# Kernel optimization log

Measured on AMD Instinct MI355X. Metric: run time of the kernel, lower is better.

Reference implementation:

```python
import jax, jax.numpy as jnp
import numpy as np

B, H, N, D = 16, 8, 256, 32


def setup_inputs() -> dict:
    key = jax.random.key(0)
    k1, k2, k3 = jax.random.split(key, 3)
    q = jax.random.normal(k1, (B, H, N, D), dtype=jnp.float32)
    k = jax.random.normal(k2, (B, H, N, D), dtype=jnp.float32)
    scale = jnp.ones((1,), dtype=jnp.float32)  # unused by the module
    mask = jnp.zeros((B, 1, N, N), dtype=bool)  # True == masked out
    # learned attention vector, xavier_uniform over (1, H, 1, 1, D)
    fan = 1 * H * 1 * 1 * D
    bound = float(np.sqrt(6.0 / (1 + D)))  # xavier for (..., D) param
    attention = jax.random.uniform(k3, (1, H, 1, 1, D), dtype=jnp.float32,
                                   minval=-bound, maxval=bound)
    return {"q": q, "k": k, "scale": scale, "mask": mask, "attention": attention}


def reference(q, k, scale, mask, attention):
    # summed: [B, H, Nq, Nk, D] via broadcast of q.unsqueeze(-2)+k.unsqueeze(-3)
    summed = q[:, :, :, None, :] + k[:, :, None, :, :]
    # GATv2 score: a^T * silu(q_i + k_j), reduced over head_dim
    scores = jnp.sum(jax.nn.silu(summed) * attention, axis=-1)  # [B, H, Nq, Nk]
    neg = jnp.finfo(scores.dtype).min
    scores_masked = jnp.where(mask, neg, scores)
    attn = jax.nn.softmax(scores_masked, axis=-1)
    return attn
```

## Files before the change

kernel.cpp:

```cpp
#include <hip/hip_runtime.h>
#include <stdint.h>
#include <stddef.h>

constexpr int Bc = 16, Hc = 8, Nc = 256, Dc = 32;
constexpr float LOG2E = 1.44269504088896340736f;

constexpr int    MF    = 10;
constexpr double PHALF = 9.7;
constexpr double LFIT  = 9.0;

constexpr double PI_ = 3.14159265358979323846;

constexpr double cexp_(double x) {
    int n = (int)(x >= 0 ? x + 0.5 : x - 0.5);
    double f = x - n, t = 1.0, s = 1.0;
    for (int i = 1; i <= 26; ++i) { t *= f / i; s += t; }
    const double E = 2.71828182845904523536;
    double en = 1.0, bb = n >= 0 ? E : 1.0 / E;
    int an = n < 0 ? -n : n;
    for (int i = 0; i < an; ++i) en *= bb;
    return s * en;
}
constexpr double creduce_(double x) {
    while (x >  PI_) x -= 2.0 * PI_;
    while (x < -PI_) x += 2.0 * PI_;
    return x;
}
constexpr double ccos_(double x0) {
    double x = creduce_(x0), x2 = x * x, t = 1.0, s = 1.0;
    for (int i = 1; i <= 16; ++i) { t *= -x2 / ((2.0*i - 1.0) * (2.0*i)); s += t; }
    return s;
}
constexpr double csin_(double x0) {
    double x = creduce_(x0), x2 = x * x, t = x, s = x;
    for (int i = 1; i <= 16; ++i) { t *= -x2 / ((2.0*i) * (2.0*i + 1.0)); s += t; }
    return s;
}
constexpr double Gfun_(double x) {
    double z = x < 0 ? -x : x;
    double e = cexp_(z);
    return 0.5 * z * ((e - 1.0) / (e + 1.0));
}
constexpr double csqrt_(double x) {
    if (x <= 0) return 0;
    double r = x > 1 ? x : 1;
    for (int i = 0; i < 40; ++i) r = 0.5 * (r + x / r);
    return r;
}

struct FitT { float tk[MF + 1]; float tq[MF + 1]; };

constexpr FitT lsFit_() {
    constexpr int NB = MF + 1;
    double A[NB][NB] = {}, bv[NB] = {};
    for (int p = 0; p < NB; ++p)
        for (int qq = 0; qq < NB; ++qq) {
            double wm = (p - qq) * PI_ / PHALF, wp = (p + qq) * PI_ / PHALF;
            double Sm = (p == qq)     ? LFIT : csin_(wm * LFIT) / wm;
            double Sp = (p + qq == 0) ? LFIT : csin_(wp * LFIT) / wp;
            A[p][qq] = 0.5 * (Sm + Sp);
        }
    constexpr int NS = 128;
    double hh = LFIT / NS, gx[NS + 1] = {};
    for (int i = 0; i <= NS; ++i) gx[i] = Gfun_(i * hh);
    for (int p = 0; p < NB; ++p) {
        double s = 0;
        for (int i = 0; i <= NS; ++i) {
            double wgt = (i == 0 || i == NS) ? 1.0 : ((i & 1) ? 4.0 : 2.0);
            s += wgt * gx[i] * ccos_(p * PI_ / PHALF * (i * hh));
        }
        bv[p] = s * hh / 3.0;
    }
    for (int p = 0; p < NB; ++p) A[p][p] += 1e-8 * LFIT;
    for (int col = 0; col < NB; ++col) {
        int piv = col; double best = A[col][col] < 0 ? -A[col][col] : A[col][col];
        for (int r = col + 1; r < NB; ++r) {
            double v = A[r][col] < 0 ? -A[r][col] : A[r][col];
            if (v > best) { best = v; piv = r; }
        }
        if (piv != col) {
            for (int cc = 0; cc < NB; ++cc) { double t = A[col][cc]; A[col][cc] = A[piv][cc]; A[piv][cc] = t; }
            double t = bv[col]; bv[col] = bv[piv]; bv[piv] = t;
        }
        for (int r = col + 1; r < NB; ++r) {
            double f = A[r][col] / A[col][col];
            for (int cc = col; cc < NB; ++cc) A[r][cc] -= f * A[col][cc];
            bv[r] -= f * bv[col];
        }
    }
    double c[NB] = {};
    for (int r = NB - 1; r >= 0; --r) {
        double s = bv[r];
        for (int cc = r + 1; cc < NB; ++cc) s -= A[r][cc] * c[cc];
        c[r] = s / A[r][r];
    }
    FitT f{};
    for (int m = 0; m <= MF; ++m) {
        double rt = csqrt_(c[m] < 0 ? -c[m] : c[m]);
        f.tk[m] = (float)rt;
        f.tq[m] = (float)(c[m] < 0 ? -rt : rt);
    }
    return f;
}
constexpr FitT CF = lsFit_();

typedef _Float16 half8  __attribute__((ext_vector_type(8)));
typedef float    f32x16 __attribute__((ext_vector_type(16)));

__device__ __forceinline__ uint32_t pkh_(float a, float b) {
    auto v = __builtin_amdgcn_cvt_pkrtz(a, b);
    uint32_t u; __builtin_memcpy(&u, &v, 4); return u;
}

constexpr int ROWB = 144;
constexpr int KB_  = Nc * ROWB;
constexpr int QB_  = 128 * ROWB;
constexpr int BUF  = KB_ + QB_;
constexpr int SRED_OFF = 2 * BUF;
constexpr int AKV_OFF  = SRED_OFF + 2048;
constexpr int SMEM     = AKV_OFF + 1024;

__global__ __launch_bounds__(512, 2) void gatv2_mfma_kernel(
    const float* __restrict__ q, const float* __restrict__ k,
    const uint8_t* __restrict__ mask, const float* __restrict__ att,
    float* __restrict__ out)
{
    extern __shared__ char smem[];
    float* sred = (float*)(smem + SRED_OFF);
    float* akv  = (float*)(smem + AKV_OFF);

    const int tid = threadIdx.x, lane = tid & 63, w = tid >> 6;
    const int bh = blockIdx.y, h = bh & 7, b = bh >> 3;
    const int iBlk = blockIdx.x * 128;
    const float invTwoP = (float)(1.0 / (2.0 * PHALF));

    const int dq = tid & 7, rw = tid >> 3;
    const float4 a4 = *(const float4*)(att + h * Dc + 4 * dq);

    const float* kbase = k + (size_t)bh * Nc * Dc;
    float kc1[16], ks1[16], kcm[16], ksm[16];
    int offK[4];
#pragma unroll
    for (int it = 0; it < 4; ++it) {
        const int j = rw + it * 64;
        const float4 kv = *(const float4*)(kbase + j * Dc + 4 * dq);
        float part = a4.x * kv.x + a4.y * kv.y + a4.z * kv.z + a4.w * kv.w;
        part += __shfl_xor(part, 1, 64);
        part += __shfl_xor(part, 2, 64);
        part += __shfl_xor(part, 4, 64);
        if (dq == 0) akv[j] = part;
        const float rv[4] = { kv.x, kv.y, kv.z, kv.w };
#pragma unroll
        for (int c = 0; c < 4; ++c) {
            float r = __builtin_amdgcn_fractf(rv[c] * invTwoP);
            kc1[4*it+c] = __builtin_amdgcn_cosf(r);
            ks1[4*it+c] = __builtin_amdgcn_sinf(r);
            kcm[4*it+c] = kc1[4*it+c];
            ksm[4*it+c] = ks1[4*it+c];
        }
        offK[it] = j * ROWB + dq * 16;
    }
    const float* qbase = q + ((size_t)bh * Nc + iBlk) * Dc;
    float qc1[8], qs1[8], qcm[8], qsm[8];
    int offQ[2];
#pragma unroll
    for (int it = 0; it < 2; ++it) {
        const int iq = rw + it * 64;
        const float4 qv = *(const float4*)(qbase + iq * Dc + 4 * dq);
        const float rv[4] = { qv.x, qv.y, qv.z, qv.w };
#pragma unroll
        for (int c = 0; c < 4; ++c) {
            float r = __builtin_amdgcn_fractf(rv[c] * invTwoP);
            qc1[4*it+c] = __builtin_amdgcn_cosf(r);
            qs1[4*it+c] = __builtin_amdgcn_sinf(r);
            qcm[4*it+c] = qc1[4*it+c];
            qsm[4*it+c] = qs1[4*it+c];
        }
        offQ[it] = KB_ + iq * ROWB + dq * 16;
    }

    const int hi5 = lane >> 5, col = lane & 31;
    const int wi = w & 1, wj = w >> 1;
    const int baseA0 = KB_ + (wi * 64 + col) * ROWB, baseA1 = baseA0 + 32 * ROWB;
    const int baseB0 = (wj * 64 + col) * ROWB,       baseB1 = baseB0 + 32 * ROWB;

    f32x16 acc[2][2];
#pragma unroll
    for (int i2 = 0; i2 < 2; ++i2)
#pragma unroll
        for (int j2 = 0; j2 < 2; ++j2)
#pragma unroll
            for (int e = 0; e < 16; ++e) acc[i2][j2][e] = 0.0f;

    auto buildWrite = [&](int mN, int dstOff) {
        const float tk = CF.tk[mN];
        const float g0 = CF.tq[mN]*a4.x, g1 = CF.tq[mN]*a4.y;
        const float g2 = CF.tq[mN]*a4.z, g3 = CF.tq[mN]*a4.w;
#pragma unroll
        for (int it = 0; it < 4; ++it) {
            uint4 wv;
            wv.x = pkh_(tk * kcm[4*it+0], tk * ksm[4*it+0]);
            wv.y = pkh_(tk * kcm[4*it+1], tk * ksm[4*it+1]);
            wv.z = pkh_(tk * kcm[4*it+2], tk * ksm[4*it+2]);
            wv.w = pkh_(tk * kcm[4*it+3], tk * ksm[4*it+3]);
            *(uint4*)(smem + dstOff + offK[it]) = wv;
        }
#pragma unroll
        for (int it = 0; it < 2; ++it) {
            uint4 wv;
            wv.x = pkh_(g0 * qcm[4*it+0], -(g0 * qsm[4*it+0]));
            wv.y = pkh_(g1 * qcm[4*it+1], -(g1 * qsm[4*it+1]));
            wv.z = pkh_(g2 * qcm[4*it+2], -(g2 * qsm[4*it+2]));
            wv.w = pkh_(g3 * qcm[4*it+3], -(g3 * qsm[4*it+3]));
            *(uint4*)(smem + dstOff + offQ[it]) = wv;
        }
    };
    auto rotate = [&]() {
#pragma unroll
        for (int e = 0; e < 16; ++e) {
            float cn = fmaf(kc1[e], kcm[e], -(ks1[e] * ksm[e]));
            float sn = fmaf(ks1[e], kcm[e],   kc1[e] * ksm[e]);
            kcm[e] = cn; ksm[e] = sn;
        }
#pragma unroll
        for (int e = 0; e < 8; ++e) {
            float cn = fmaf(qc1[e], qcm[e], -(qs1[e] * qsm[e]));
            float sn = fmaf(qs1[e], qcm[e],   qc1[e] * qsm[e]);
            qcm[e] = cn; qsm[e] = sn;
        }
    };
    auto loadFrags = [&](int srcOff, int s, half8& A0, half8& A1,
                         half8& B0, half8& B1) {
        const int du = (2 * s + hi5) << 4;
        A0 = *(const half8*)(smem + srcOff + baseA0 + du);
        A1 = *(const half8*)(smem + srcOff + baseA1 + du);
        B0 = *(const half8*)(smem + srcOff + baseB0 + du);
        B1 = *(const half8*)(smem + srcOff + baseB1 + du);
    };
    auto mfma4 = [&](half8 A0, half8 A1, half8 B0, half8 B1) {
        acc[0][0] = __builtin_amdgcn_mfma_f32_32x32x16_f16(A0, B0, acc[0][0], 0, 0, 0);
        acc[0][1] = __builtin_amdgcn_mfma_f32_32x32x16_f16(A0, B1, acc[0][1], 0, 0, 0);
        acc[1][0] = __builtin_amdgcn_mfma_f32_32x32x16_f16(A1, B0, acc[1][0], 0, 0, 0);
        acc[1][1] = __builtin_amdgcn_mfma_f32_32x32x16_f16(A1, B1, acc[1][1], 0, 0, 0);
    };

    buildWrite(1, 0);
    rotate();
    __syncthreads();
#pragma unroll
    for (int m = 1; m <= MF; ++m) {
        const int srcOff = ((m - 1) & 1) * BUF;
        const int dstOff = (m & 1) * BUF;
        half8 A0a, A1a, B0a, B1a, A0b, A1b, B0b, B1b;
        loadFrags(srcOff, 0, A0a, A1a, B0a, B1a);
        loadFrags(srcOff, 1, A0b, A1b, B0b, B1b);
        if (m < MF) { buildWrite(m + 1, dstOff); rotate(); }
        __builtin_amdgcn_s_setprio(1);
        mfma4(A0a, A1a, B0a, B1a);
        loadFrags(srcOff, 2, A0a, A1a, B0a, B1a);
        mfma4(A0b, A1b, B0b, B1b);
        loadFrags(srcOff, 3, A0b, A1b, B0b, B1b);
        mfma4(A0a, A1a, B0a, B1a);
        mfma4(A0b, A1b, B0b, B1b);
        __builtin_amdgcn_s_setprio(0);
        if (m < MF) __syncthreads();
    }

    constexpr float M0 = 24.0f;
    const int jB = wj * 64;
    const float akj0 = akv[jB + col], akj1 = akv[jB + 32 + col];
    const int iB = iBlk + wi * 64;

#pragma unroll
    for (int i2 = 0; i2 < 2; ++i2) {
        float v[16];
#pragma unroll
        for (int e = 0; e < 16; ++e) {
            const int rloc = (e & 3) + 8 * (e >> 2) + 4 * hi5;
            const int ig = iB + i2 * 32 + rloc;
            const uint8_t* mr = mask + ((size_t)(b * Nc + ig)) * Nc + jB + col;
            const uint8_t m0 = mr[0], m1 = mr[32];
            float v0 = fmaf(0.5f, akj0, acc[i2][0][e]);
            float v1 = fmaf(0.5f, akj1, acc[i2][1][e]);
            float p0 = __builtin_amdgcn_exp2f(__builtin_fminf((v0 - M0) * LOG2E, 80.0f));
            float p1 = __builtin_amdgcn_exp2f(__builtin_fminf((v1 - M0) * LOG2E, 80.0f));
            if (m0) p0 = 0.0f;
            if (m1) p1 = 0.0f;
            acc[i2][0][e] = p0;
            acc[i2][1][e] = p1;
            v[e] = p0 + p1;
        }
        float u8[8];
#pragma unroll
        for (int jj = 0; jj < 8; ++jj) {
            float mn = (col & 16) ? v[jj + 8] : v[jj];
            float sd = (col & 16) ? v[jj]     : v[jj + 8];
            u8[jj] = mn + __shfl_xor(sd, 16, 64);
        }
        float u4[4];
#pragma unroll
        for (int jj = 0; jj < 4; ++jj) {
            float mn = (col & 8) ? u8[jj + 4] : u8[jj];
            float sd = (col & 8) ? u8[jj]     : u8[jj + 4];
            u4[jj] = mn + __shfl_xor(sd, 8, 64);
        }
        float u2[2];
#pragma unroll
        for (int jj = 0; jj < 2; ++jj) {
            float mn = (col & 4) ? u4[jj + 2] : u4[jj];
            float sd = (col & 4) ? u4[jj]     : u4[jj + 2];
            u2[jj] = mn + __shfl_xor(sd, 4, 64);
        }
        float t1;
        {
            float mn = (col & 2) ? u2[1] : u2[0];
            float sd = (col & 2) ? u2[0] : u2[1];
            t1 = mn + __shfl_xor(sd, 2, 64);
        }
        t1 += __shfl_xor(t1, 1, 64);
        {
            const int eL = ((col & 16) ? 8 : 0) + ((col & 8) ? 4 : 0)
                         + ((col & 4) ? 2 : 0) + ((col & 2) ? 1 : 0);
            const int rl = (eL & 3) + 8 * (eL >> 2) + 4 * hi5;
            if (!(col & 1)) sred[(wi * 64 + i2 * 32 + rl) * 4 + wj] = t1;
        }
    }
    __syncthreads();

    float* obase = out + (size_t)bh * Nc * Nc;
#pragma unroll
    for (int i2 = 0; i2 < 2; ++i2)
#pragma unroll
    for (int e = 0; e < 16; ++e) {
        const int rloc = (e & 3) + 8 * (e >> 2) + 4 * hi5;
        const int iL = wi * 64 + i2 * 32 + rloc;
        const int ig = iBlk + iL;
        const float4 tv = *(const float4*)(&sred[iL * 4]);
        const float inv = __builtin_amdgcn_rcpf(tv.x + tv.y + tv.z + tv.w);
        obase[(size_t)ig * Nc + jB + col]      = acc[i2][0][e] * inv;
        obase[(size_t)ig * Nc + jB + 32 + col] = acc[i2][1][e] * inv;
    }
}

extern "C" void kernel_launch(void* const* d_in, const int* in_sizes, int n_in,
                              void* d_out, int out_size, void* d_ws, size_t ws_size,
                              hipStream_t stream) {
    const float*   q    = (const float*)d_in[0];
    const float*   k    = (const float*)d_in[1];
    const uint8_t* mask = (const uint8_t*)d_in[3];
    const float*   att  = (const float*)d_in[4];
    float*         out  = (float*)d_out;

    (void)hipFuncSetAttribute((const void*)gatv2_mfma_kernel,
                              hipFuncAttributeMaxDynamicSharedMemorySize, SMEM);

    dim3 grid(2, Bc * Hc);
    dim3 block(512);
    gatv2_mfma_kernel<<<grid, block, SMEM, stream>>>(q, k, mask, att, out);
}
```

Measured before the change: 91.38 us.

## Split block into producer waves building Fourier features and MFMA consumer waves

Adds four producer waves to each block (768 threads). The producers compute the cos/sin feature tiles for every harmonic and write them into the double-buffered LDS, while the original eight waves only run the MFMA loop and the softmax epilogue. The producers no longer advance the features with the incremental angle-rotation recurrence; they recompute cos/sin directly from a stored phase on each harmonic. The aim is to take feature generation off the MFMA waves' critical path. In exchange it raises the thread count and register pressure under launch_bounds(768,3), uses more transcendental instructions, and still synchronises with a block barrier on every harmonic.

```diff
diff --git a/kernel.cpp b/kernel.cpp
--- a/kernel.cpp
+++ b/kernel.cpp
@@ -120,7 +120,7 @@
 constexpr int AKV_OFF  = SRED_OFF + 2048;
 constexpr int SMEM     = AKV_OFF + 1024;
 
-__global__ __launch_bounds__(512, 2) void gatv2_mfma_kernel(
+__global__ __launch_bounds__(768, 3) void gatv2_mfma_kernel(
     const float* __restrict__ q, const float* __restrict__ k,
     const uint8_t* __restrict__ mask, const float* __restrict__ att,
     float* __restrict__ out)
@@ -133,100 +133,94 @@
     const int bh = blockIdx.y, h = bh & 7, b = bh >> 3;
     const int iBlk = blockIdx.x * 128;
     const float invTwoP = (float)(1.0 / (2.0 * PHALF));
-
-    const int dq = tid & 7, rw = tid >> 3;
-    const float4 a4 = *(const float4*)(att + h * Dc + 4 * dq);
-
-    const float* kbase = k + (size_t)bh * Nc * Dc;
-    float kc1[16], ks1[16], kcm[16], ksm[16];
-    int offK[4];
-#pragma unroll
-    for (int it = 0; it < 4; ++it) {
-        const int j = rw + it * 64;
-        const float4 kv = *(const float4*)(kbase + j * Dc + 4 * dq);
-        float part = a4.x * kv.x + a4.y * kv.y + a4.z * kv.z + a4.w * kv.w;
-        part += __shfl_xor(part, 1, 64);
-        part += __shfl_xor(part, 2, 64);
-        part += __shfl_xor(part, 4, 64);
-        if (dq == 0) akv[j] = part;
-        const float rv[4] = { kv.x, kv.y, kv.z, kv.w };
-#pragma unroll
-        for (int c = 0; c < 4; ++c) {
-            float r = __builtin_amdgcn_fractf(rv[c] * invTwoP);
-            kc1[4*it+c] = __builtin_amdgcn_cosf(r);
-            ks1[4*it+c] = __builtin_amdgcn_sinf(r);
-            kcm[4*it+c] = kc1[4*it+c];
-            ksm[4*it+c] = ks1[4*it+c];
-        }
-        offK[it] = j * ROWB + dq * 16;
-    }
-    const float* qbase = q + ((size_t)bh * Nc + iBlk) * Dc;
-    float qc1[8], qs1[8], qcm[8], qsm[8];
-    int offQ[2];
-#pragma unroll
-    for (int it = 0; it < 2; ++it) {
-        const int iq = rw + it * 64;
-        const float4 qv = *(const float4*)(qbase + iq * Dc + 4 * dq);
-        const float rv[4] = { qv.x, qv.y, qv.z, qv.w };
-#pragma unroll
-        for (int c = 0; c < 4; ++c) {
-            float r = __builtin_amdgcn_fractf(rv[c] * invTwoP);
-            qc1[4*it+c] = __builtin_amdgcn_cosf(r);
-            qs1[4*it+c] = __builtin_amdgcn_sinf(r);
-            qcm[4*it+c] = qc1[4*it+c];
-            qsm[4*it+c] = qs1[4*it+c];
-        }
-        offQ[it] = KB_ + iq * ROWB + dq * 16;
-    }
+    const bool isProd = (w >= 8);
+
+    float kph[32], qph[16];
+    int offK[8], offQ[4];
+    float4 a4p{0,0,0,0};
 
     const int hi5 = lane >> 5, col = lane & 31;
-    const int wi = w & 1, wj = w >> 1;
+    const int wi = w & 1, wj = (w >> 1) & 3;
     const int baseA0 = KB_ + (wi * 64 + col) * ROWB, baseA1 = baseA0 + 32 * ROWB;
     const int baseB0 = (wj * 64 + col) * ROWB,       baseB1 = baseB0 + 32 * ROWB;
 
     f32x16 acc[2][2];
-#pragma unroll
-    for (int i2 = 0; i2 < 2; ++i2)
-#pragma unroll
-        for (int j2 = 0; j2 < 2; ++j2)
-#pragma unroll
-            for (int e = 0; e < 16; ++e) acc[i2][j2][e] = 0.0f;
+
+    if (isProd) {
+        const int p = tid - 512, dq = p & 7, rw = p >> 3;
+        a4p = *(const float4*)(att + h * Dc + 4 * dq);
+        const float* kbase = k + (size_t)bh * Nc * Dc;
+#pragma unroll
+        for (int it = 0; it < 8; ++it) {
+            const int j = rw + it * 32;
+            const float4 kv = *(const float4*)(kbase + j * Dc + 4 * dq);
+            float part = a4p.x * kv.x + a4p.y * kv.y + a4p.z * kv.z + a4p.w * kv.w;
+            part += __shfl_xor(part, 1, 64);
+            part += __shfl_xor(part, 2, 64);
+            part += __shfl_xor(part, 4, 64);
+            if (dq == 0) akv[j] = part;
+            kph[4*it+0] = __builtin_amdgcn_fractf(kv.x * invTwoP);
+            kph[4*it+1] = __builtin_amdgcn_fractf(kv.y * invTwoP);
+            kph[4*it+2] = __builtin_amdgcn_fractf(kv.z * invTwoP);
+            kph[4*it+3] = __builtin_amdgcn_fractf(kv.w * invTwoP);
+            offK[it] = j * ROWB + dq * 16;
+        }
+        const float* qbase = q + ((size_t)bh * Nc + iBlk) * Dc;
+#pragma unroll
+        for (int it = 0; it < 4; ++it) {
+            const int iq = rw + it * 32;
+            const float4 qv = *(const float4*)(qbase + iq * Dc + 4 * dq);
+            qph[4*it+0] = __builtin_amdgcn_fractf(qv.x * invTwoP);
+            qph[4*it+1] = __builtin_amdgcn_fractf(qv.y * invTwoP);
+            qph[4*it+2] = __builtin_amdgcn_fractf(qv.z * invTwoP);
+            qph[4*it+3] = __builtin_amdgcn_fractf(qv.w * invTwoP);
+            offQ[it] = KB_ + iq * ROWB + dq * 16;
+        }
+    } else {
+#pragma unroll
+        for (int i2 = 0; i2 < 2; ++i2)
+#pragma unroll
+            for (int j2 = 0; j2 < 2; ++j2)
+#pragma unroll
+                for (int e = 0; e < 16; ++e) acc[i2][j2][e] = 0.0f;
+    }
 
     auto buildWrite = [&](int mN, int dstOff) {
+        const float mf = (float)mN;
         const float tk = CF.tk[mN];
-        const float g0 = CF.tq[mN]*a4.x, g1 = CF.tq[mN]*a4.y;
-        const float g2 = CF.tq[mN]*a4.z, g3 = CF.tq[mN]*a4.w;
+        const float g0 = CF.tq[mN]*a4p.x, g1 = CF.tq[mN]*a4p.y;
+        const float g2 = CF.tq[mN]*a4p.z, g3 = CF.tq[mN]*a4p.w;
+#pragma unroll
+        for (int it = 0; it < 8; ++it) {
+            float cs[4], sn[4];
+#pragma unroll
+            for (int c = 0; c < 4; ++c) {
+                const float r = __builtin_amdgcn_fractf(mf * kph[4*it+c]);
+                cs[c] = __builtin_amdgcn_cosf(r);
+                sn[c] = __builtin_amdgcn_sinf(r);
+            }
+            uint4 wv;
+            wv.x = pkh_(tk * cs[0], tk * sn[0]);
+            wv.y = pkh_(tk * cs[1], tk * sn[1]);
+            wv.z = pkh_(tk * cs[2], tk * sn[2]);
+            wv.w = pkh_(tk * cs[3], tk * sn[3]);
+            *(uint4*)(smem + dstOff + offK[it]) = wv;
+        }
 #pragma unroll
         for (int it = 0; it < 4; ++it) {
+            float cs[4], sn[4];
+#pragma unroll
+            for (int c = 0; c < 4; ++c) {
+                const float r = __builtin_amdgcn_fractf(mf * qph[4*it+c]);
+                cs[c] = __builtin_amdgcn_cosf(r);
+                sn[c] = __builtin_amdgcn_sinf(r);
+            }
             uint4 wv;
-            wv.x = pkh_(tk * kcm[4*it+0], tk * ksm[4*it+0]);
-            wv.y = pkh_(tk * kcm[4*it+1], tk * ksm[4*it+1]);
-            wv.z = pkh_(tk * kcm[4*it+2], tk * ksm[4*it+2]);
-            wv.w = pkh_(tk * kcm[4*it+3], tk * ksm[4*it+3]);
-            *(uint4*)(smem + dstOff + offK[it]) = wv;
-        }
-#pragma unroll
-        for (int it = 0; it < 2; ++it) {
-            uint4 wv;
-            wv.x = pkh_(g0 * qcm[4*it+0], -(g0 * qsm[4*it+0]));
-            wv.y = pkh_(g1 * qcm[4*it+1], -(g1 * qsm[4*it+1]));
-            wv.z = pkh_(g2 * qcm[4*it+2], -(g2 * qsm[4*it+2]));
-            wv.w = pkh_(g3 * qcm[4*it+3], -(g3 * qsm[4*it+3]));
+            wv.x = pkh_(g0 * cs[0], -(g0 * sn[0]));
+            wv.y = pkh_(g1 * cs[1], -(g1 * sn[1]));
+            wv.z = pkh_(g2 * cs[2], -(g2 * sn[2]));
+            wv.w = pkh_(g3 * cs[3], -(g3 * sn[3]));
             *(uint4*)(smem + dstOff + offQ[it]) = wv;
-        }
-    };
-    auto rotate = [&]() {
-#pragma unroll
-        for (int e = 0; e < 16; ++e) {
-            float cn = fmaf(kc1[e], kcm[e], -(ks1[e] * ksm[e]));
-            float sn = fmaf(ks1[e], kcm[e],   kc1[e] * ksm[e]);
-            kcm[e] = cn; ksm[e] = sn;
-        }
-#pragma unroll
-        for (int e = 0; e < 8; ++e) {
-            float cn = fmaf(qc1[e], qcm[e], -(qs1[e] * qsm[e]));
-            float sn = fmaf(qs1[e], qcm[e],   qc1[e] * qsm[e]);
-            qcm[e] = cn; qsm[e] = sn;
         }
     };
     auto loadFrags = [&](int srcOff, int s, half8& A0, half8& A1,
@@ -244,101 +238,106 @@
         acc[1][1] = __builtin_amdgcn_mfma_f32_32x32x16_f16(A1, B1, acc[1][1], 0, 0, 0);
     };
 
-    buildWrite(1, 0);
-    rotate();
+    if (isProd) buildWrite(1, 0);
     __syncthreads();
 #pragma unroll
     for (int m = 1; m <= MF; ++m) {
-        const int srcOff = ((m - 1) & 1) * BUF;
-        const int dstOff = (m & 1) * BUF;
-        half8 A0a, A1a, B0a, B1a, A0b, A1b, B0b, B1b;
-        loadFrags(srcOff, 0, A0a, A1a, B0a, B1a);
-        loadFrags(srcOff, 1, A0b, A1b, B0b, B1b);
-        if (m < MF) { buildWrite(m + 1, dstOff); rotate(); }
-        __builtin_amdgcn_s_setprio(1);
-        mfma4(A0a, A1a, B0a, B1a);
-        loadFrags(srcOff, 2, A0a, A1a, B0a, B1a);
-        mfma4(A0b, A1b, B0b, B1b);
-        loadFrags(srcOff, 3, A0b, A1b, B0b, B1b);
-        mfma4(A0a, A1a, B0a, B1a);
-        mfma4(A0b, A1b, B0b, B1b);
-        __builtin_amdgcn_s_setprio(0);
+        if (!isProd) {
+            const int srcOff = ((m - 1) & 1) * BUF;
+            half8 A0a, A1a, B0a, B1a, A0b, A1b, B0b, B1b;
+            loadFrags(srcOff, 0, A0a, A1a, B0a, B1a);
+            loadFrags(srcOff, 1, A0b, A1b, B0b, B1b);
+            __builtin_amdgcn_s_setprio(1);
+            mfma4(A0a, A1a, B0a, B1a);
+            loadFrags(srcOff, 2, A0a, A1a, B0a, B1a);
+            mfma4(A0b, A1b, B0b, B1b);
+            loadFrags(srcOff, 3, A0b, A1b, B0b, B1b);
+            mfma4(A0a, A1a, B0a, B1a);
+            mfma4(A0b, A1b, B0b, B1b);
+            __builtin_amdgcn_s_setprio(0);
+        } else if (m < MF) {
+            buildWrite(m + 1, (m & 1) * BUF);
+        }
         if (m < MF) __syncthreads();
     }
 
     constexpr float M0 = 24.0f;
     const int jB = wj * 64;
-    const float akj0 = akv[jB + col], akj1 = akv[jB + 32 + col];
     const int iB = iBlk + wi * 64;
 
-#pragma unroll
-    for (int i2 = 0; i2 < 2; ++i2) {
-        float v[16];
+    if (!isProd) {
+        const float akj0 = akv[jB + col], akj1 = akv[jB + 32 + col];
+#pragma unroll
+        for (int i2 = 0; i2 < 2; ++i2) {
+            float v[16];
+#pragma unroll
+            for (int e = 0; e < 16; ++e) {
+                const int rloc = (e & 3) + 8 * (e >> 2) + 4 * hi5;
+                const int ig = iB + i2 * 32 + rloc;
+                const uint8_t* mr = mask + ((size_t)(b * Nc + ig)) * Nc + jB + col;
+                const uint8_t m0 = mr[0], m1 = mr[32];
+                float v0 = fmaf(0.5f, akj0, acc[i2][0][e]);
+                float v1 = fmaf(0.5f, akj1, acc[i2][1][e]);
+                float p0 = __builtin_amdgcn_exp2f(__builtin_fminf((v0 - M0) * LOG2E, 80.0f));
+                float p1 = __builtin_amdgcn_exp2f(__builtin_fminf((v1 - M0) * LOG2E, 80.0f));
+                if (m0) p0 = 0.0f;
+                if (m1) p1 = 0.0f;
+                acc[i2][0][e] = p0;
+                acc[i2][1][e] = p1;
+                v[e] = p0 + p1;
+            }
+            float u8[8];
+#pragma unroll
+            for (int jj = 0; jj < 8; ++jj) {
+                float mn = (col & 16) ? v[jj + 8] : v[jj];
+                float sd = (col & 16) ? v[jj]     : v[jj + 8];
+                u8[jj] = mn + __shfl_xor(sd, 16, 64);
+            }
+            float u4[4];
+#pragma unroll
+            for (int jj = 0; jj < 4; ++jj) {
+                float mn = (col & 8) ? u8[jj + 4] : u8[jj];
+                float sd = (col & 8) ? u8[jj]     : u8[jj + 4];
+                u4[jj] = mn + __shfl_xor(sd, 8, 64);
+            }
+            float u2[2];
+#pragma unroll
+            for (int jj = 0; jj < 2; ++jj) {
+                float mn = (col & 4) ? u4[jj + 2] : u4[jj];
+                float sd = (col & 4) ? u4[jj]     : u4[jj + 2];
+                u2[jj] = mn + __shfl_xor(sd, 4, 64);
+            }
+            float t1;
+            {
+                float mn = (col & 2) ? u2[1] : u2[0];
+                float sd = (col & 2) ? u2[0] : u2[1];
+                t1 = mn + __shfl_xor(sd, 2, 64);
+            }
+            t1 += __shfl_xor(t1, 1, 64);
+            {
+                const int eL = ((col & 16) ? 8 : 0) + ((col & 8) ? 4 : 0)
+                             + ((col & 4) ? 2 : 0) + ((col & 2) ? 1 : 0);
+                const int rl = (eL & 3) + 8 * (eL >> 2) + 4 * hi5;
+                if (!(col & 1)) sred[(wi * 64 + i2 * 32 + rl) * 4 + wj] = t1;
+            }
+        }
+    }
+    __syncthreads();
+
+    if (!isProd) {
+        float* obase = out + (size_t)bh * Nc * Nc;
+#pragma unroll
+        for (int i2 = 0; i2 < 2; ++i2)
 #pragma unroll
         for (int e = 0; e < 16; ++e) {
             const int rloc = (e & 3) + 8 * (e >> 2) + 4 * hi5;
-            const int ig = iB + i2 * 32 + rloc;
-            const uint8_t* mr = mask + ((size_t)(b * Nc + ig)) * Nc + jB + col;
-            const uint8_t m0 = mr[0], m1 = mr[32];
-            float v0 = fmaf(0.5f, akj0, acc[i2][0][e]);
-            float v1 = fmaf(0.5f, akj1, acc[i2][1][e]);
-            float p0 = __builtin_amdgcn_exp2f(__builtin_fminf((v0 - M0) * LOG2E, 80.0f));
-            float p1 = __builtin_amdgcn_exp2f(__builtin_fminf((v1 - M0) * LOG2E, 80.0f));
-            if (m0) p0 = 0.0f;
-            if (m1) p1 = 0.0f;
-            acc[i2][0][e] = p0;
-            acc[i2][1][e] = p1;
-            v[e] = p0 + p1;
-        }
-        float u8[8];
-#pragma unroll
-        for (int jj = 0; jj < 8; ++jj) {
-            float mn = (col & 16) ? v[jj + 8] : v[jj];
-            float sd = (col & 16) ? v[jj]     : v[jj + 8];
-            u8[jj] = mn + __shfl_xor(sd, 16, 64);
-        }
-        float u4[4];
-#pragma unroll
-        for (int jj = 0; jj < 4; ++jj) {
-            float mn = (col & 8) ? u8[jj + 4] : u8[jj];
-            float sd = (col & 8) ? u8[jj]     : u8[jj + 4];
-            u4[jj] = mn + __shfl_xor(sd, 8, 64);
-        }
-        float u2[2];
-#pragma unroll
-        for (int jj = 0; jj < 2; ++jj) {
-            float mn = (col & 4) ? u4[jj + 2] : u4[jj];
-            float sd = (col & 4) ? u4[jj]     : u4[jj + 2];
-            u2[jj] = mn + __shfl_xor(sd, 4, 64);
-        }
-        float t1;
-        {
-            float mn = (col & 2) ? u2[1] : u2[0];
-            float sd = (col & 2) ? u2[0] : u2[1];
-            t1 = mn + __shfl_xor(sd, 2, 64);
-        }
-        t1 += __shfl_xor(t1, 1, 64);
-        {
-            const int eL = ((col & 16) ? 8 : 0) + ((col & 8) ? 4 : 0)
-                         + ((col & 4) ? 2 : 0) + ((col & 2) ? 1 : 0);
-            const int rl = (eL & 3) + 8 * (eL >> 2) + 4 * hi5;
-            if (!(col & 1)) sred[(wi * 64 + i2 * 32 + rl) * 4 + wj] = t1;
-        }
-    }
-    __syncthreads();
-
-    float* obase = out + (size_t)bh * Nc * Nc;
-#pragma unroll
-    for (int i2 = 0; i2 < 2; ++i2)
-#pragma unroll
-    for (int e = 0; e < 16; ++e) {
-        const int rloc = (e & 3) + 8 * (e >> 2) + 4 * hi5;
-        const int iL = wi * 64 + i2 * 32 + rloc;
-        const int ig = iBlk + iL;
-        const float4 tv = *(const float4*)(&sred[iL * 4]);
-        const float inv = __builtin_amdgcn_rcpf(tv.x + tv.y + tv.z + tv.w);
-        obase[(size_t)ig * Nc + jB + col]      = acc[i2][0][e] * inv;
-        obase[(size_t)ig * Nc + jB + 32 + col] = acc[i2][1][e] * inv;
+            const int iL = wi * 64 + i2 * 32 + rloc;
+            const int ig = iBlk + iL;
+            const float4 tv = *(const float4*)(&sred[iL * 4]);
+            const float inv = __builtin_amdgcn_rcpf(tv.x + tv.y + tv.z + tv.w);
+            obase[(size_t)ig * Nc + jB + col]      = acc[i2][0][e] * inv;
+            obase[(size_t)ig * Nc + jB + 32 + col] = acc[i2][1][e] * inv;
+        }
     }
 }
 
@@ -355,6 +354,6 @@
                               hipFuncAttributeMaxDynamicSharedMemorySize, SMEM);
 
     dim3 grid(2, Bc * Hc);
-    dim3 block(512);
+    dim3 block(768);
     gatv2_mfma_kernel<<<grid, block, SMEM, stream>>>(q, k, mask, att, out);
 }
```

New measurement: 96.13 us. +5.2%, slower.

## Warp-specialize into producer waves building fragments and consumer MFMA waves

Applied to the files above, without the earlier changes.

Doubles the block to 1024 threads and splits it by role. Waves 8-15 compute the sin/cos features and write the fp16 operand buffers for the next Fourier term, while waves 0-7 only load fragments, run MFMA, and do the softmax epilogue. The aim is to overlap the VALU-heavy feature construction with the matrix work on separate waves instead of interleaving both in one instruction stream. In exchange, launch_bounds(1024,4) tightens the per-thread register budget (spill risk) and producers and consumers still meet at a barrier every iteration.

```diff
diff --git a/kernel.cpp b/kernel.cpp
--- a/kernel.cpp
+++ b/kernel.cpp
@@ -120,7 +120,7 @@
 constexpr int AKV_OFF  = SRED_OFF + 2048;
 constexpr int SMEM     = AKV_OFF + 1024;
 
-__global__ __launch_bounds__(512, 2) void gatv2_mfma_kernel(
+__global__ __launch_bounds__(1024, 4) void gatv2_mfma_kernel(
     const float* __restrict__ q, const float* __restrict__ k,
     const uint8_t* __restrict__ mask, const float* __restrict__ att,
     float* __restrict__ out)
@@ -133,69 +133,73 @@
     const int bh = blockIdx.y, h = bh & 7, b = bh >> 3;
     const int iBlk = blockIdx.x * 128;
     const float invTwoP = (float)(1.0 / (2.0 * PHALF));
-
-    const int dq = tid & 7, rw = tid >> 3;
-    const float4 a4 = *(const float4*)(att + h * Dc + 4 * dq);
-
-    const float* kbase = k + (size_t)bh * Nc * Dc;
+    const bool isProd = (w >= 8);
+
     float kc1[16], ks1[16], kcm[16], ksm[16];
-    int offK[4];
-#pragma unroll
-    for (int it = 0; it < 4; ++it) {
-        const int j = rw + it * 64;
-        const float4 kv = *(const float4*)(kbase + j * Dc + 4 * dq);
-        float part = a4.x * kv.x + a4.y * kv.y + a4.z * kv.z + a4.w * kv.w;
-        part += __shfl_xor(part, 1, 64);
-        part += __shfl_xor(part, 2, 64);
-        part += __shfl_xor(part, 4, 64);
-        if (dq == 0) akv[j] = part;
-        const float rv[4] = { kv.x, kv.y, kv.z, kv.w };
-#pragma unroll
-        for (int c = 0; c < 4; ++c) {
-            float r = __builtin_amdgcn_fractf(rv[c] * invTwoP);
-            kc1[4*it+c] = __builtin_amdgcn_cosf(r);
-            ks1[4*it+c] = __builtin_amdgcn_sinf(r);
-            kcm[4*it+c] = kc1[4*it+c];
-            ksm[4*it+c] = ks1[4*it+c];
-        }
-        offK[it] = j * ROWB + dq * 16;
-    }
-    const float* qbase = q + ((size_t)bh * Nc + iBlk) * Dc;
     float qc1[8], qs1[8], qcm[8], qsm[8];
-    int offQ[2];
-#pragma unroll
-    for (int it = 0; it < 2; ++it) {
-        const int iq = rw + it * 64;
-        const float4 qv = *(const float4*)(qbase + iq * Dc + 4 * dq);
-        const float rv[4] = { qv.x, qv.y, qv.z, qv.w };
-#pragma unroll
-        for (int c = 0; c < 4; ++c) {
-            float r = __builtin_amdgcn_fractf(rv[c] * invTwoP);
-            qc1[4*it+c] = __builtin_amdgcn_cosf(r);
-            qs1[4*it+c] = __builtin_amdgcn_sinf(r);
-            qcm[4*it+c] = qc1[4*it+c];
-            qsm[4*it+c] = qs1[4*it+c];
-        }
-        offQ[it] = KB_ + iq * ROWB + dq * 16;
-    }
+    int offK[4], offQ[2];
+    float4 a4p{0,0,0,0};
 
     const int hi5 = lane >> 5, col = lane & 31;
-    const int wi = w & 1, wj = w >> 1;
+    const int wi = w & 1, wj = (w >> 1) & 3;
     const int baseA0 = KB_ + (wi * 64 + col) * ROWB, baseA1 = baseA0 + 32 * ROWB;
     const int baseB0 = (wj * 64 + col) * ROWB,       baseB1 = baseB0 + 32 * ROWB;
 
     f32x16 acc[2][2];
-#pragma unroll
-    for (int i2 = 0; i2 < 2; ++i2)
-#pragma unroll
-        for (int j2 = 0; j2 < 2; ++j2)
-#pragma unroll
-            for (int e = 0; e < 16; ++e) acc[i2][j2][e] = 0.0f;
+
+    if (isProd) {
+        const int p = tid - 512, dq = p & 7, rw = p >> 3;
+        a4p = *(const float4*)(att + h * Dc + 4 * dq);
+        const float* kbase = k + (size_t)bh * Nc * Dc;
+#pragma unroll
+        for (int it = 0; it < 4; ++it) {
+            const int j = rw + it * 64;
+            const float4 kv = *(const float4*)(kbase + j * Dc + 4 * dq);
+            float part = a4p.x * kv.x + a4p.y * kv.y + a4p.z * kv.z + a4p.w * kv.w;
+            part += __shfl_xor(part, 1, 64);
+            part += __shfl_xor(part, 2, 64);
+            part += __shfl_xor(part, 4, 64);
+            if (dq == 0) akv[j] = part;
+            const float rv[4] = { kv.x, kv.y, kv.z, kv.w };
+#pragma unroll
+            for (int c = 0; c < 4; ++c) {
+                float r = __builtin_amdgcn_fractf(rv[c] * invTwoP);
+                kc1[4*it+c] = __builtin_amdgcn_cosf(r);
+                ks1[4*it+c] = __builtin_amdgcn_sinf(r);
+                kcm[4*it+c] = kc1[4*it+c];
+                ksm[4*it+c] = ks1[4*it+c];
+            }
+            offK[it] = j * ROWB + dq * 16;
+        }
+        const float* qbase = q + ((size_t)bh * Nc + iBlk) * Dc;
+#pragma unroll
+        for (int it = 0; it < 2; ++it) {
+            const int iq = rw + it * 64;
+            const float4 qv = *(const float4*)(qbase + iq * Dc + 4 * dq);
+            const float rv[4] = { qv.x, qv.y, qv.z, qv.w };
+#pragma unroll
+            for (int c = 0; c < 4; ++c) {
+                float r = __builtin_amdgcn_fractf(rv[c] * invTwoP);
+                qc1[4*it+c] = __builtin_amdgcn_cosf(r);
+                qs1[4*it+c] = __builtin_amdgcn_sinf(r);
+                qcm[4*it+c] = qc1[4*it+c];
+                qsm[4*it+c] = qs1[4*it+c];
+            }
+            offQ[it] = KB_ + iq * ROWB + dq * 16;
+        }
+    } else {
+#pragma unroll
+        for (int i2 = 0; i2 < 2; ++i2)
+#pragma unroll
+            for (int j2 = 0; j2 < 2; ++j2)
+#pragma unroll
+                for (int e = 0; e < 16; ++e) acc[i2][j2][e] = 0.0f;
+    }
 
     auto buildWrite = [&](int mN, int dstOff) {
         const float tk = CF.tk[mN];
-        const float g0 = CF.tq[mN]*a4.x, g1 = CF.tq[mN]*a4.y;
-        const float g2 = CF.tq[mN]*a4.z, g3 = CF.tq[mN]*a4.w;
+        const float g0 = CF.tq[mN]*a4p.x, g1 = CF.tq[mN]*a4p.y;
+        const float g2 = CF.tq[mN]*a4p.z, g3 = CF.tq[mN]*a4p.w;
 #pragma unroll
         for (int it = 0; it < 4; ++it) {
             uint4 wv;
@@ -244,101 +248,108 @@
         acc[1][1] = __builtin_amdgcn_mfma_f32_32x32x16_f16(A1, B1, acc[1][1], 0, 0, 0);
     };
 
-    buildWrite(1, 0);
-    rotate();
+    if (isProd) buildWrite(1, 0);
+    if (isProd) rotate();
     __syncthreads();
 #pragma unroll
     for (int m = 1; m <= MF; ++m) {
-        const int srcOff = ((m - 1) & 1) * BUF;
-        const int dstOff = (m & 1) * BUF;
-        half8 A0a, A1a, B0a, B1a, A0b, A1b, B0b, B1b;
-        loadFrags(srcOff, 0, A0a, A1a, B0a, B1a);
-        loadFrags(srcOff, 1, A0b, A1b, B0b, B1b);
-        if (m < MF) { buildWrite(m + 1, dstOff); rotate(); }
-        __builtin_amdgcn_s_setprio(1);
-        mfma4(A0a, A1a, B0a, B1a);
-        loadFrags(srcOff, 2, A0a, A1a, B0a, B1a);
-        mfma4(A0b, A1b, B0b, B1b);
-        loadFrags(srcOff, 3, A0b, A1b, B0b, B1b);
-        mfma4(A0a, A1a, B0a, B1a);
-        mfma4(A0b, A1b, B0b, B1b);
-        __builtin_amdgcn_s_setprio(0);
+        if (!isProd) {
+            const int srcOff = ((m - 1) & 1) * BUF;
+            half8 A0a, A1a, B0a, B1a, A0b, A1b, B0b, B1b;
+            loadFrags(srcOff, 0, A0a, A1a, B0a, B1a);
+            loadFrags(srcOff, 1, A0b, A1b, B0b, B1b);
+            __builtin_amdgcn_s_setprio(1);
+            mfma4(A0a, A1a, B0a, B1a);
+            loadFrags(srcOff, 2, A0a, A1a, B0a, B1a);
+            mfma4(A0b, A1b, B0b, B1b);
+            loadFrags(srcOff, 3, A0b, A1b, B0b, B1b);
+            mfma4(A0a, A1a, B0a, B1a);
+            mfma4(A0b, A1b, B0b, B1b);
+            __builtin_amdgcn_s_setprio(0);
+        } else if (m < MF) {
+            buildWrite(m + 1, (m & 1) * BUF);
+            rotate();
+        }
         if (m < MF) __syncthreads();
     }
 
     constexpr float M0 = 24.0f;
     const int jB = wj * 64;
-    const float akj0 = akv[jB + col], akj1 = akv[jB + 32 + col];
     const int iB = iBlk + wi * 64;
 
-#pragma unroll
-    for (int i2 = 0; i2 < 2; ++i2) {
-        float v[16];
+    if (!isProd) {
+        const float akj0 = akv[jB + col], akj1 = akv[jB + 32 + col];
+#pragma unroll
+        for (int i2 = 0; i2 < 2; ++i2) {
+            float v[16];
+#pragma unroll
+            for (int e = 0; e < 16; ++e) {
+                const int rloc = (e & 3) + 8 * (e >> 2) + 4 * hi5;
+                const int ig = iB + i2 * 32 + rloc;
+                const uint8_t* mr = mask + ((size_t)(b * Nc + ig)) * Nc + jB + col;
+                const uint8_t m0 = mr[0], m1 = mr[32];
+                float v0 = fmaf(0.5f, akj0, acc[i2][0][e]);
+                float v1 = fmaf(0.5f, akj1, acc[i2][1][e]);
+                float p0 = __builtin_amdgcn_exp2f(__builtin_fminf((v0 - M0) * LOG2E, 80.0f));
+                float p1 = __builtin_amdgcn_exp2f(__builtin_fminf((v1 - M0) * LOG2E, 80.0f));
+                if (m0) p0 = 0.0f;
+                if (m1) p1 = 0.0f;
+                acc[i2][0][e] = p0;
+                acc[i2][1][e] = p1;
+                v[e] = p0 + p1;
+            }
+            float u8[8];
+#pragma unroll
+            for (int jj = 0; jj < 8; ++jj) {
+                float mn = (col & 16) ? v[jj + 8] : v[jj];
+                float sd = (col & 16) ? v[jj]     : v[jj + 8];
+                u8[jj] = mn + __shfl_xor(sd, 16, 64);
+            }
+            float u4[4];
+#pragma unroll
+            for (int jj = 0; jj < 4; ++jj) {
+                float mn = (col & 8) ? u8[jj + 4] : u8[jj];
+                float sd = (col & 8) ? u8[jj]     : u8[jj + 4];
+                u4[jj] = mn + __shfl_xor(sd, 8, 64);
+            }
+            float u2[2];
+#pragma unroll
+            for (int jj = 0; jj < 2; ++jj) {
+                float mn = (col & 4) ? u4[jj + 2] : u4[jj];
+                float sd = (col & 4) ? u4[jj]     : u4[jj + 2];
+                u2[jj] = mn + __shfl_xor(sd, 4, 64);
+            }
+            float t1;
+            {
+                float mn = (col & 2) ? u2[1] : u2[0];
+                float sd = (col & 2) ? u2[0] : u2[1];
+                t1 = mn + __shfl_xor(sd, 2, 64);
+            }
+            t1 += __shfl_xor(t1, 1, 64);
+            {
+                const int eL = ((col & 16) ? 8 : 0) + ((col & 8) ? 4 : 0)
+                             + ((col & 4) ? 2 : 0) + ((col & 2) ? 1 : 0);
+                const int rl = (eL & 3) + 8 * (eL >> 2) + 4 * hi5;
+                if (!(col & 1)) sred[(wi * 64 + i2 * 32 + rl) * 4 + wj] = t1;
+            }
+        }
+    }
+    __syncthreads();
+
+    if (!isProd) {
+        float* obase = out + (size_t)bh * Nc * Nc;
+#pragma unroll
+        for (int i2 = 0; i2 < 2; ++i2)
 #pragma unroll
         for (int e = 0; e < 16; ++e) {
             const int rloc = (e & 3) + 8 * (e >> 2) + 4 * hi5;
-            const int ig = iB + i2 * 32 + rloc;
-            const uint8_t* mr = mask + ((size_t)(b * Nc + ig)) * Nc + jB + col;
-            const uint8_t m0 = mr[0], m1 = mr[32];
-            float v0 = fmaf(0.5f, akj0, acc[i2][0][e]);
-            float v1 = fmaf(0.5f, akj1, acc[i2][1][e]);
-            float p0 = __builtin_amdgcn_exp2f(__builtin_fminf((v0 - M0) * LOG2E, 80.0f));
-            float p1 = __builtin_amdgcn_exp2f(__builtin_fminf((v1 - M0) * LOG2E, 80.0f));
-            if (m0) p0 = 0.0f;
-            if (m1) p1 = 0.0f;
-            acc[i2][0][e] = p0;
-            acc[i2][1][e] = p1;
-            v[e] = p0 + p1;
-        }
-        float u8[8];
-#pragma unroll
-        for (int jj = 0; jj < 8; ++jj) {
-            float mn = (col & 16) ? v[jj + 8] : v[jj];
-            float sd = (col & 16) ? v[jj]     : v[jj + 8];
-            u8[jj] = mn + __shfl_xor(sd, 16, 64);
-        }
-        float u4[4];
-#pragma unroll
-        for (int jj = 0; jj < 4; ++jj) {
-            float mn = (col & 8) ? u8[jj + 4] : u8[jj];
-            float sd = (col & 8) ? u8[jj]     : u8[jj + 4];
-            u4[jj] = mn + __shfl_xor(sd, 8, 64);
-        }
-        float u2[2];
-#pragma unroll
-        for (int jj = 0; jj < 2; ++jj) {
-            float mn = (col & 4) ? u4[jj + 2] : u4[jj];
-            float sd = (col & 4) ? u4[jj]     : u4[jj + 2];
-            u2[jj] = mn + __shfl_xor(sd, 4, 64);
-        }
-        float t1;
-        {
-            float mn = (col & 2) ? u2[1] : u2[0];
-            float sd = (col & 2) ? u2[0] : u2[1];
-            t1 = mn + __shfl_xor(sd, 2, 64);
-        }
-        t1 += __shfl_xor(t1, 1, 64);
-        {
-            const int eL = ((col & 16) ? 8 : 0) + ((col & 8) ? 4 : 0)
-                         + ((col & 4) ? 2 : 0) + ((col & 2) ? 1 : 0);
-            const int rl = (eL & 3) + 8 * (eL >> 2) + 4 * hi5;
-            if (!(col & 1)) sred[(wi * 64 + i2 * 32 + rl) * 4 + wj] = t1;
-        }
-    }
-    __syncthreads();
-
-    float* obase = out + (size_t)bh * Nc * Nc;
-#pragma unroll
-    for (int i2 = 0; i2 < 2; ++i2)
-#pragma unroll
-    for (int e = 0; e < 16; ++e) {
-        const int rloc = (e & 3) + 8 * (e >> 2) + 4 * hi5;
-        const int iL = wi * 64 + i2 * 32 + rloc;
-        const int ig = iBlk + iL;
-        const float4 tv = *(const float4*)(&sred[iL * 4]);
-        const float inv = __builtin_amdgcn_rcpf(tv.x + tv.y + tv.z + tv.w);
-        obase[(size_t)ig * Nc + jB + col]      = acc[i2][0][e] * inv;
-        obase[(size_t)ig * Nc + jB + 32 + col] = acc[i2][1][e] * inv;
+            const int iL = wi * 64 + i2 * 32 + rloc;
+            const int ig = iBlk + iL;
+            const float4 tv = *(const float4*)(&sred[iL * 4]);
+            const float inv = __builtin_amdgcn_rcpf(tv.x + tv.y + tv.z + tv.w);
+            obase[(size_t)ig * Nc + jB + col]      = acc[i2][0][e] * inv;
+            obase[(size_t)ig * Nc + jB + 32 + col] = acc[i2][1][e] * inv;
+        }
     }
 }
 
@@ -355,6 +366,6 @@
                               hipFuncAttributeMaxDynamicSharedMemorySize, SMEM);
 
     dim3 grid(2, Bc * Hc);
-    dim3 block(512);
+    dim3 block(1024);
     gatv2_mfma_kernel<<<grid, block, SMEM, stream>>>(q, k, mask, att, out);
 }
```

New measurement: 206.9 us. 126% more time.
